# Performance work log

Hardware: AMD Instinct MI355X
Metric: run time of the kernel (lower is better)

The kernel has to match this reference:

```python
import jax, jax.numpy as jnp
import numpy as np

N = 51200      # total nodes
E = 1638400    # total edges (avg degree 32)
G = 512        # graphs in batch
IN = 16        # input node features
H = 4          # heads
C = 32         # channels per head
HC = H * C     # 128, concat output width
SLOPE = 0.2    # LeakyReLU negative slope
BN_EPS = 1e-5


def _glorot(k, shape, fan):
    return jax.random.normal(k, shape, jnp.float32) / np.sqrt(fan).astype(np.float32)


def setup_inputs() -> dict:
    key = jax.random.key(0)
    ks = jax.random.split(key, 32)
    inp = {}
    inp['x'] = jax.random.normal(ks[0], (N, IN), jnp.float32)
    inp['edge_index'] = jax.random.randint(ks[1], (2, E), 0, N)
    inp['batch'] = jnp.sort(jax.random.randint(ks[2], (N,), 0, G))
    # GATv2 layer 1 (IN -> H*C)
    inp['l1_Wl'] = _glorot(ks[3], (IN, HC), IN)
    inp['l1_bl'] = jnp.zeros((HC,), jnp.float32)
    inp['l1_Wr'] = _glorot(ks[4], (IN, HC), IN)
    inp['l1_br'] = jnp.zeros((HC,), jnp.float32)
    inp['l1_att'] = _glorot(ks[5], (H, C), C)
    inp['l1_bias'] = jnp.zeros((HC,), jnp.float32)
    # GATv2 layer 2 (HC -> H*C)
    inp['l2_Wl'] = _glorot(ks[6], (HC, HC), HC)
    inp['l2_bl'] = jnp.zeros((HC,), jnp.float32)
    inp['l2_Wr'] = _glorot(ks[7], (HC, HC), HC)
    inp['l2_br'] = jnp.zeros((HC,), jnp.float32)
    inp['l2_att'] = _glorot(ks[8], (H, C), C)
    inp['l2_bias'] = jnp.zeros((HC,), jnp.float32)
    # MLP head (HC -> HC -> HC -> 2) with BatchNorm (eval mode, running stats 0/1)
    inp['fc1_W'] = _glorot(ks[9], (HC, HC), HC)
    inp['fc1_b'] = jnp.zeros((HC,), jnp.float32)
    inp['bn1_g'] = jnp.ones((HC,), jnp.float32)
    inp['bn1_b'] = jnp.zeros((HC,), jnp.float32)
    inp['fc2_W'] = _glorot(ks[10], (HC, HC), HC)
    inp['fc2_b'] = jnp.zeros((HC,), jnp.float32)
    inp['bn2_g'] = jnp.ones((HC,), jnp.float32)
    inp['bn2_b'] = jnp.zeros((HC,), jnp.float32)
    inp['fc3_W'] = _glorot(ks[11], (HC, 2), HC)
    inp['fc3_b'] = jnp.zeros((2,), jnp.float32)
    return inp


def gatv2_conv(x, src, dst, Wl, bl, Wr, br, att, bias):
    # PyG GATv2Conv (share_weights=False, concat=True), eval mode (no dropout).
    xl = (x @ Wl + bl).reshape(-1, H, C)  # source transform  [N,H,C]
    xr = (x @ Wr + br).reshape(-1, H, C)  # target transform  [N,H,C]
    e = jax.nn.leaky_relu(xl[src] + xr[dst], SLOPE)   # [E,H,C]
    score = jnp.einsum('ehc,hc->eh', e, att)          # [E,H]
    # segment softmax over edges sharing the same target node
    m = jax.ops.segment_max(score, dst, num_segments=N)
    ex = jnp.exp(score - m[dst])
    denom = jax.ops.segment_sum(ex, dst, num_segments=N)
    alpha = ex / (denom[dst] + 1e-16)                 # [E,H]
    out = jax.ops.segment_sum(xl[src] * alpha[:, :, None], dst, num_segments=N)
    return out.reshape(-1, HC) + bias


def reference(x, edge_index, batch,
              l1_Wl, l1_bl, l1_Wr, l1_br, l1_att, l1_bias,
              l2_Wl, l2_bl, l2_Wr, l2_br, l2_att, l2_bias,
              fc1_W, fc1_b, bn1_g, bn1_b,
              fc2_W, fc2_b, bn2_g, bn2_b,
              fc3_W, fc3_b):
    src, dst = edge_index[0], edge_index[1]
    h = jax.nn.relu(gatv2_conv(x, src, dst, l1_Wl, l1_bl, l1_Wr, l1_br, l1_att, l1_bias))
    h = jax.nn.relu(gatv2_conv(h, src, dst, l2_Wl, l2_bl, l2_Wr, l2_br, l2_att, l2_bias))
    # global mean pool over graphs
    s = jax.ops.segment_sum(h, batch, num_segments=G)
    cnt = jax.ops.segment_sum(jnp.ones((N,), h.dtype), batch, num_segments=G)
    g = s / jnp.maximum(cnt, 1.0)[:, None]            # [G,HC]
    # MLP head; BatchNorm1d in eval mode with running_mean=0, running_var=1
    def bn(z, gamma, beta):
        return z * (gamma / np.sqrt(1.0 + BN_EPS).astype(np.float32)) + beta
    g = jax.nn.relu(bn(g @ fc1_W + fc1_b, bn1_g, bn1_b))
    g = jax.nn.relu(bn(g @ fc2_W + fc2_b, bn2_g, bn2_b))
    return g @ fc3_W + fc3_b                          # [G,2]
```

## Files before the change

### kernel.cpp

```cpp
#include <hip/hip_runtime.h>
#include <math.h>

#define NN 51200
#define EE 1638400
#define GG 512
#define INF 16
#define HCC 128
#define NB 400
#define TILE 4096
#define NBLK (NN / 4)

typedef float vf2 __attribute__((ext_vector_type(2)));
#define FMA2 __builtin_elementwise_fma
#define MIN2 __builtin_elementwise_min
#define MAX2 __builtin_elementwise_max


__device__ __forceinline__ int wave_incl_scan(int v, int lane) {
#pragma unroll
    for (int d = 1; d < 64; d <<= 1) {
        int y = __shfl_up(v, d);
        if (lane >= d) v += y;
    }
    return v;
}

__global__ __launch_bounds__(256) void k_hist(const int* __restrict__ ei,
                                              int* __restrict__ bcnt) {
    __shared__ int h[NB];
    for (int i = threadIdx.x; i < NB; i += 256) h[i] = 0;
    __syncthreads();
    int e0 = blockIdx.x * TILE;
#pragma unroll
    for (int s = 0; s < 16; s++) {
        int d = ei[EE + e0 + s * 256 + threadIdx.x];
        atomicAdd(&h[d >> 7], 1);
    }
    __syncthreads();
    for (int i = threadIdx.x; i < NB; i += 256)
        if (h[i]) atomicAdd(&bcnt[i], h[i]);
}

__global__ __launch_bounds__(512) void k_scan2(const int* __restrict__ bcnt,
                                               int* __restrict__ bbase,
                                               int* __restrict__ gcur,
                                               int* __restrict__ rowptr) {
    __shared__ int sc[512];
    int t = threadIdx.x;
    int v = (t < NB) ? bcnt[t] : 0;
    sc[t] = v;
    __syncthreads();
    for (int off = 1; off < 512; off <<= 1) {
        int u = (t >= off) ? sc[t - off] : 0;
        __syncthreads();
        sc[t] += u;
        __syncthreads();
    }
    if (t < NB) { int ex = sc[t] - v; bbase[t] = ex; gcur[t] = ex; }
    if (t == 0) { bbase[NB] = EE; rowptr[NN] = EE; }
}

__global__ __launch_bounds__(512) void k_binlin1(const int* __restrict__ ei,
                                                 int* __restrict__ gcur,
                                                 unsigned* __restrict__ binned,
                                                 const float* __restrict__ x,
                                                 const float* __restrict__ Wl,
                                                 const float* __restrict__ bl,
                                                 const float* __restrict__ Wr,
                                                 const float* __restrict__ br,
                                                 float* __restrict__ xl,
                                                 float* __restrict__ xr) {
    __shared__ int h[512];
    __shared__ int lexcl[NB], lcur[NB], baseg[NB];
    __shared__ unsigned stage[TILE];
    __shared__ int wsum[8];
    __shared__ float sx[4][INF];
    int t = threadIdx.x;
    if (blockIdx.x < NB) {
        int lane = t & 63, w = t >> 6;
        h[t] = 0;
        __syncthreads();
        int e0 = blockIdx.x * TILE;
        int sv[8], dv[8];
#pragma unroll
        for (int s = 0; s < 8; s++) {
            int e = e0 + s * 512 + t;
            sv[s] = ei[e];
            dv[s] = ei[EE + e];
            atomicAdd(&h[dv[s] >> 7], 1);
        }
        __syncthreads();
        int myh = h[t];
        int incl = wave_incl_scan(myh, lane);
        if (lane == 63) wsum[w] = incl;
        __syncthreads();
        int woff = 0;
        for (int i = 0; i < w; i++) woff += wsum[i];
        incl += woff;
        if (t < NB) {
            int ex = incl - myh;
            lexcl[t] = ex;
            lcur[t] = ex;
            baseg[t] = atomicAdd(&gcur[t], myh);
        }
        __syncthreads();
#pragma unroll
        for (int s = 0; s < 8; s++) {
            int b = dv[s] >> 7;
            int r = atomicAdd(&lcur[b], 1);
            stage[r] = (unsigned)sv[s] | ((unsigned)dv[s] << 16);
        }
        __syncthreads();
#pragma unroll
        for (int s = 0; s < 8; s++) {
            int idx = s * 512 + t;
            unsigned p = stage[idx];
            int b = (int)(p >> 23);
            binned[baseg[b] + idx - lexcl[b]] = p;
        }
    } else {
        int bid = blockIdx.x - NB;
        int j = t & 127;
        int ty = t >> 7;
        int row = bid * 4 + ty;
        if (t < 64) {
            sx[t >> 4][t & 15] = x[(size_t)(bid * 4 + (t >> 4)) * INF + (t & 15)];
        }
        __syncthreads();
        float al = bl[j], ar = br[j];
#pragma unroll
        for (int k = 0; k < INF; k++) {
            float xv = sx[ty][k];
            al = fmaf(xv, Wl[k * HCC + j], al);
            ar = fmaf(xv, Wr[k * HCC + j], ar);
        }
        size_t s = ((size_t)(j >> 5) * NN + row) * 32 + (j & 31);
        xl[s] = al;
        xr[s] = ar;
    }
}

__global__ __launch_bounds__(256) void k_csr(const unsigned* __restrict__ binned,
                                             const int* __restrict__ bbase,
                                             int* __restrict__ rowptr,
                                             int* __restrict__ col) {
    int b = blockIdx.x;
    int base = bbase[b];
    int cnt = bbase[b + 1] - base;
    __shared__ int nh[1024], ncur[1024];
    __shared__ int wsum[4];
    int t = threadIdx.x;
    int lane = t & 63, w = t >> 6;
#pragma unroll
    for (int i = 0; i < 4; i++) nh[t + 256 * i] = 0;
    __syncthreads();
    for (int e = t; e < cnt; e += 256) {
        unsigned p = binned[base + e];
        unsigned src = p & 0xFFFFu;
        int key = (int)(((p >> 16) & 127u) << 3) | (int)(src >> 13);
        atomicAdd(&nh[key], 1);
    }
    __syncthreads();
    int c0 = nh[4 * t + 0], c1 = nh[4 * t + 1], c2 = nh[4 * t + 2], c3 = nh[4 * t + 3];
    int tot = ((c0 + c1) + (c2 + c3));
    int incl = wave_incl_scan(tot, lane);
    if (lane == 63) wsum[w] = incl;
    __syncthreads();
    int woff = 0;
    for (int i = 0; i < w; i++) woff += wsum[i];
    int tex = incl + woff - tot;
    ncur[4 * t + 0] = base + tex;
    ncur[4 * t + 1] = base + tex + c0;
    ncur[4 * t + 2] = base + tex + c0 + c1;
    ncur[4 * t + 3] = base + tex + c0 + c1 + c2;
    if ((t & 1) == 0) rowptr[(b << 7) + (t >> 1)] = base + tex;
    __syncthreads();
    for (int e = t; e < cnt; e += 256) {
        unsigned p = binned[base + e];
        unsigned src = p & 0xFFFFu;
        int key = (int)(((p >> 16) & 127u) << 3) | (int)(src >> 13);
        int r = atomicAdd(&ncur[key], 1);
        col[r] = (int)src;
    }
}

#define AST2 36
#define BST 260
__global__ __launch_bounds__(512) void k_lin2(const float* __restrict__ hin,
                                              const float* __restrict__ Wl,
                                              const float* __restrict__ bl,
                                              const float* __restrict__ Wr,
                                              const float* __restrict__ br,
                                              float* __restrict__ outl,
                                              float* __restrict__ outr) {
    __shared__ float As[128 * AST2];
    __shared__ float Bs[32 * BST];
    const int tid = threadIdx.x;
    const int cx = tid & 31;
    const int cy = tid >> 5;
    const int r0 = blockIdx.x * 128;

    vf2 accL[8][2], accR[8][2];
#pragma unroll
    for (int j = 0; j < 8; j++)
#pragma unroll
        for (int i = 0; i < 2; i++) {
            accL[j][i] = (vf2){0.f, 0.f};
            accR[j][i] = (vf2){0.f, 0.f};
        }

    for (int k0 = 0; k0 < HCC; k0 += 32) {
#pragma unroll
        for (int s = 0; s < 2; s++) {
            int f = tid + 512 * s;
            int row = f >> 3;
            int kk = (f & 7) * 4;
            float4 v = *(const float4*)(hin + (size_t)(r0 + row) * HCC + k0 + kk);
            *(float4*)&As[row * AST2 + kk] = v;
        }
#pragma unroll
        for (int s = 0; s < 4; s++) {
            int g = tid + 512 * s;
            int kr = g >> 6;
            int c4 = g & 63;
            const float* srcp = (c4 < 32)
                ? (Wl + (size_t)(k0 + kr) * HCC + c4 * 4)
                : (Wr + (size_t)(k0 + kr) * HCC + (c4 - 32) * 4);
            *(float4*)&Bs[kr * BST + c4 * 4] = *(const float4*)srcp;
        }
        __syncthreads();
#pragma unroll
        for (int k = 0; k < 32; k += 4) {
            float4 a4[8];
#pragma unroll
            for (int j = 0; j < 8; ++j)
                a4[j] = *(const float4*)&As[(cy + 16 * j) * AST2 + k];
#pragma unroll
            for (int kk = 0; kk < 4; ++kk) {
                float4 b4l = *(const float4*)&Bs[(k + kk) * BST + cx * 4];
                float4 b4r = *(const float4*)&Bs[(k + kk) * BST + 128 + cx * 4];
                const vf2 bl0 = {b4l.x, b4l.y}, bl1 = {b4l.z, b4l.w};
                const vf2 br0 = {b4r.x, b4r.y}, br1 = {b4r.z, b4r.w};
#pragma unroll
                for (int j = 0; j < 8; ++j) {
                    float a = ((const float*)&a4[j])[kk];
                    const vf2 av = {a, a};
                    accL[j][0] = FMA2(av, bl0, accL[j][0]);
                    accL[j][1] = FMA2(av, bl1, accL[j][1]);
                    accR[j][0] = FMA2(av, br0, accR[j][0]);
                    accR[j][1] = FMA2(av, br1, accR[j][1]);
                }
            }
        }
        __syncthreads();
    }
    float4 bv_l = *(const float4*)(bl + cx * 4);
    float4 bv_r = *(const float4*)(br + cx * 4);
    const size_t plane = (size_t)(cx >> 3) * NN * 32;
    const int off = (cx & 7) * 4;
#pragma unroll
    for (int j = 0; j < 8; ++j) {
        int row = r0 + cy + 16 * j;
        float4 o;
        o.x = accL[j][0].x + bv_l.x;
        o.y = accL[j][0].y + bv_l.y;
        o.z = accL[j][1].x + bv_l.z;
        o.w = accL[j][1].y + bv_l.w;
        *(float4*)(outl + plane + (size_t)row * 32 + off) = o;
        o.x = accR[j][0].x + bv_r.x;
        o.y = accR[j][0].y + bv_r.y;
        o.z = accR[j][1].x + bv_r.z;
        o.w = accR[j][1].y + bv_r.w;
        *(float4*)(outr + plane + (size_t)row * 32 + off) = o;
    }
}

__global__ __launch_bounds__(256) void k_attn(const int* __restrict__ rowptr,
                                              const int* __restrict__ col,
                                              const float* __restrict__ xl,
                                              const float* __restrict__ xr,
                                              const float* __restrict__ att,
                                              const float* __restrict__ bias,
                                              float* __restrict__ hout) {
    const int wave = threadIdx.x >> 6;
    const int lane = threadIdx.x & 63;
    const int sub = lane >> 3;
    const int hl = (lane >> 2) & 1;
    const int hq = lane & 3;
    const int pair = blockIdx.x / NBLK;
    const int n = (blockIdx.x - pair * NBLK) * 4 + wave;
    const int head = 2 * pair + hl;

    const float* xlh = xl + (size_t)head * NN * 32;
    const float* xrp = xr + ((size_t)head * NN + n) * 32 + hq * 8;
    const float4 xrv0 = *(const float4*)(xrp);
    const float4 xrv1 = *(const float4*)(xrp + 4);
    const float4 at0 = *(const float4*)(att + head * 32 + hq * 8);
    const float4 at1 = *(const float4*)(att + head * 32 + hq * 8 + 4);
    const vf2 xr01 = {xrv0.x, xrv0.y}, xr23 = {xrv0.z, xrv0.w};
    const vf2 xr45 = {xrv1.x, xrv1.y}, xr67 = {xrv1.z, xrv1.w};
    const vf2 at01 = {at0.x, at0.y}, at23 = {at0.z, at0.w};
    const vf2 at45 = {at1.x, at1.y}, at67 = {at1.z, at1.w};
    const vf2 Z2 = {0.f, 0.f}, C2 = {0.2f, 0.2f};
    const unsigned choff = (unsigned)hq * 32u;

    const int base = rowptr[n];
    const int deg = rowptr[n + 1] - base;

    float m = -INFINITY, l = 0.f;
    vf2 a01 = Z2, a23 = Z2, a45 = Z2, a67 = Z2;

    for (int i0 = 0; i0 < deg; i0 += 64) {
        int mye = 0;
        if (i0 + lane < deg) mye = col[base + i0 + lane];
        const int cnt = min(64, deg - i0);
        const int events = (cnt + 15) >> 4;
        for (int g = 0; g < events; ++g) {
            float4 v0[2], v1[2];
            float p[2];
#pragma unroll
            for (int k = 0; k < 2; ++k) {
                const int src = __shfl(mye, 16 * g + 8 * k + sub);
                const unsigned voff = ((unsigned)src << 7) + choff;
                v0[k] = *(const float4*)((const char*)xlh + voff);
                v1[k] = *(const float4*)((const char*)xlh + voff + 16);
            }
#pragma unroll
            for (int k = 0; k < 2; ++k) {
                const vf2 v01 = {v0[k].x, v0[k].y}, v23 = {v0[k].z, v0[k].w};
                const vf2 v45 = {v1[k].x, v1[k].y}, v67 = {v1[k].z, v1[k].w};
                vf2 e, kk, p2;
                e = v01 + xr01; kk = FMA2(C2, MIN2(e, Z2), MAX2(e, Z2)); p2 = kk * at01;
                e = v23 + xr23; kk = FMA2(C2, MIN2(e, Z2), MAX2(e, Z2)); p2 = FMA2(kk, at23, p2);
                e = v45 + xr45; kk = FMA2(C2, MIN2(e, Z2), MAX2(e, Z2)); p2 = FMA2(kk, at45, p2);
                e = v67 + xr67; kk = FMA2(C2, MIN2(e, Z2), MAX2(e, Z2)); p2 = FMA2(kk, at67, p2);
                float pp = p2.x + p2.y;
                pp += __shfl_xor(pp, 1);
                pp += __shfl_xor(pp, 2);
                if ((16 * g + 8 * k + sub) >= cnt) pp = -INFINITY;
                p[k] = pp;
            }
            float pm = fmaxf(p[0], p[1]);
            pm = fmaxf(pm, __shfl_xor(pm, 8));
            pm = fmaxf(pm, __shfl_xor(pm, 16));
            pm = fmaxf(pm, __shfl_xor(pm, 32));
            const float mn = fmaxf(m, pm);
            const float sc = __expf(m - mn);
            const float w0 = __expf(p[0] - mn);
            const float w1 = __expf(p[1] - mn);
            l = fmaf(l, sc, w0 + w1);
            const vf2 S = {sc, sc}, W0 = {w0, w0}, W1 = {w1, w1};
            const vf2 u01 = {v0[0].x, v0[0].y}, u23 = {v0[0].z, v0[0].w};
            const vf2 u45 = {v1[0].x, v1[0].y}, u67 = {v1[0].z, v1[0].w};
            const vf2 t01 = {v0[1].x, v0[1].y}, t23 = {v0[1].z, v0[1].w};
            const vf2 t45 = {v1[1].x, v1[1].y}, t67 = {v1[1].z, v1[1].w};
            a01 = FMA2(W1, t01, FMA2(W0, u01, a01 * S));
            a23 = FMA2(W1, t23, FMA2(W0, u23, a23 * S));
            a45 = FMA2(W1, t45, FMA2(W0, u45, a45 * S));
            a67 = FMA2(W1, t67, FMA2(W0, u67, a67 * S));
            m = mn;
        }
    }
    l += __shfl_xor(l, 8);
    l += __shfl_xor(l, 16);
    l += __shfl_xor(l, 32);
    float af[8] = {a01.x, a01.y, a23.x, a23.y, a45.x, a45.y, a67.x, a67.y};
#pragma unroll
    for (int i = 0; i < 8; i++) {
        af[i] += __shfl_xor(af[i], 8);
        af[i] += __shfl_xor(af[i], 16);
        af[i] += __shfl_xor(af[i], 32);
    }
    const float inv = 1.f / (l + 1e-16f);
    if (sub == 0) {
        const float4 b0 = *(const float4*)(bias + head * 32 + hq * 8);
        const float4 b1 = *(const float4*)(bias + head * 32 + hq * 8 + 4);
        float4 o0, o1;
        o0.x = fmaxf(fmaf(af[0], inv, b0.x), 0.f);
        o0.y = fmaxf(fmaf(af[1], inv, b0.y), 0.f);
        o0.z = fmaxf(fmaf(af[2], inv, b0.z), 0.f);
        o0.w = fmaxf(fmaf(af[3], inv, b0.w), 0.f);
        o1.x = fmaxf(fmaf(af[4], inv, b1.x), 0.f);
        o1.y = fmaxf(fmaf(af[5], inv, b1.y), 0.f);
        o1.z = fmaxf(fmaf(af[6], inv, b1.z), 0.f);
        o1.w = fmaxf(fmaf(af[7], inv, b1.w), 0.f);
        float* hp = hout + (size_t)n * HCC + head * 32 + hq * 8;
        *(float4*)(hp) = o0;
        *(float4*)(hp + 4) = o1;
    }
}

__global__ __launch_bounds__(128) void k_head(const float* __restrict__ h,
                                              const int* __restrict__ batch,
                                              const float* __restrict__ fc1W, const float* __restrict__ fc1b,
                                              const float* __restrict__ bn1g, const float* __restrict__ bn1b,
                                              const float* __restrict__ fc2W, const float* __restrict__ fc2b,
                                              const float* __restrict__ bn2g, const float* __restrict__ bn2b,
                                              const float* __restrict__ fc3W, const float* __restrict__ fc3b,
                                              float* __restrict__ out) {
    int g = blockIdx.x;
    int j = threadIdx.x;
    __shared__ float buf[HCC], buf2[HCC];
    int lo = 0, hi = NN;
    while (lo < hi) { int mid = (lo + hi) >> 1; if (batch[mid] < g) lo = mid + 1; else hi = mid; }
    int s = lo;
    lo = 0; hi = NN;
    while (lo < hi) { int mid = (lo + hi) >> 1; if (batch[mid] < g + 1) lo = mid + 1; else hi = mid; }
    int e = lo;
    float s0 = 0.f, s1 = 0.f, s2 = 0.f, s3 = 0.f;
    int n = s;
    for (; n + 3 < e; n += 4) {
        s0 += h[(size_t)n * HCC + j];
        s1 += h[(size_t)(n + 1) * HCC + j];
        s2 += h[(size_t)(n + 2) * HCC + j];
        s3 += h[(size_t)(n + 3) * HCC + j];
    }
    for (; n < e; n++) s0 += h[(size_t)n * HCC + j];
    float sum = (s0 + s1) + (s2 + s3);
    float cnt = (float)(e - s);
    buf[j] = sum / fmaxf(cnt, 1.0f);
    __syncthreads();
    const float SQ = 1.00000499998749994f;
    float a = fc1b[j];
    for (int k = 0; k < HCC; k++) a = fmaf(buf[k], fc1W[k * HCC + j], a);
    a = fmaf(a, bn1g[j] / SQ, bn1b[j]);
    a = fmaxf(a, 0.f);
    buf2[j] = a;
    __syncthreads();
    a = fc2b[j];
    for (int k = 0; k < HCC; k++) a = fmaf(buf2[k], fc2W[k * HCC + j], a);
    a = fmaf(a, bn2g[j] / SQ, bn2b[j]);
    a = fmaxf(a, 0.f);
    buf[j] = a;
    __syncthreads();
    if (j < 2) {
        float o = fc3b[j];
        for (int k = 0; k < HCC; k++) o = fmaf(buf[k], fc3W[k * 2 + j], o);
        out[g * 2 + j] = o;
    }
}

extern "C" void kernel_launch(void* const* d_in, const int* in_sizes, int n_in,
                              void* d_out, int out_size, void* d_ws, size_t ws_size,
                              hipStream_t stream) {
    const float* x      = (const float*)d_in[0];
    const int*   ei     = (const int*)d_in[1];
    const int*   batch  = (const int*)d_in[2];
    const float* l1_Wl  = (const float*)d_in[3];
    const float* l1_bl  = (const float*)d_in[4];
    const float* l1_Wr  = (const float*)d_in[5];
    const float* l1_br  = (const float*)d_in[6];
    const float* l1_att = (const float*)d_in[7];
    const float* l1_bias= (const float*)d_in[8];
    const float* l2_Wl  = (const float*)d_in[9];
    const float* l2_bl  = (const float*)d_in[10];
    const float* l2_Wr  = (const float*)d_in[11];
    const float* l2_br  = (const float*)d_in[12];
    const float* l2_att = (const float*)d_in[13];
    const float* l2_bias= (const float*)d_in[14];
    const float* fc1_W  = (const float*)d_in[15];
    const float* fc1_b  = (const float*)d_in[16];
    const float* bn1_g  = (const float*)d_in[17];
    const float* bn1_b  = (const float*)d_in[18];
    const float* fc2_W  = (const float*)d_in[19];
    const float* fc2_b  = (const float*)d_in[20];
    const float* bn2_g  = (const float*)d_in[21];
    const float* bn2_b  = (const float*)d_in[22];
    const float* fc3_W  = (const float*)d_in[23];
    const float* fc3_b  = (const float*)d_in[24];
    float* out = (float*)d_out;

    float* xl = (float*)d_ws;
    float* xr = xl + (size_t)NN * HCC;
    float* h  = xr + (size_t)NN * HCC;
    int* rowptr = (int*)(h + (size_t)NN * HCC);
    int* col    = rowptr + (NN + 1);
    int* bcnt   = col + EE;
    int* bbase  = bcnt + NB;
    int* gcur   = bbase + (NB + 1);
    unsigned* binned = (unsigned*)h;

    hipMemsetAsync(bcnt, 0, NB * sizeof(int), stream);
    k_hist<<<EE / TILE, 256, 0, stream>>>(ei, bcnt);
    k_scan2<<<1, 512, 0, stream>>>(bcnt, bbase, gcur, rowptr);
    k_binlin1<<<NB + NN / 4, 512, 0, stream>>>(ei, gcur, binned,
                                               x, l1_Wl, l1_bl, l1_Wr, l1_br, xl, xr);
    k_csr<<<NB, 256, 0, stream>>>(binned, bbase, rowptr, col);

    k_attn<<<2 * NBLK, 256, 0, stream>>>(rowptr, col, xl, xr, l1_att, l1_bias, h);

    k_lin2<<<NN / 128, 512, 0, stream>>>(h, l2_Wl, l2_bl, l2_Wr, l2_br, xl, xr);
    k_attn<<<2 * NBLK, 256, 0, stream>>>(rowptr, col, xl, xr, l2_att, l2_bias, h);

    k_head<<<GG, 128, 0, stream>>>(h, batch, fc1_W, fc1_b, bn1_g, bn1_b,
                                   fc2_W, fc2_b, bn2_g, bn2_b, fc3_W, fc3_b, out);
}
```

Baseline: 474.6 us.

## Run layer-2 linear on bf16x3 MFMA with weights pre-split in binning kernel

Replaces the FP32 SIMT GEMM for the layer-2 source/target transforms with MFMA 16x16x32 bf16 instructions. Accuracy is kept close to FP32 by splitting each operand into hi/lo bf16 parts and summing three products. The weight split and swizzle into MFMA fragment layout happen in 8 extra blocks appended to the binning kernel, so k_lin2 reads pre-packed B fragments. The cost is a small precision change and per-element strided scalar output stores, in exchange for much higher matrix throughput on a GEMM of about 51200x128x256.

```diff
diff --git a/kernel.cpp b/kernel.cpp
--- a/kernel.cpp
+++ b/kernel.cpp
@@ -11,6 +11,8 @@
 #define NBLK (NN / 4)
 
 typedef float vf2 __attribute__((ext_vector_type(2)));
+typedef short v8s __attribute__((ext_vector_type(8)));
+typedef float v4f __attribute__((ext_vector_type(4)));
 #define FMA2 __builtin_elementwise_fma
 #define MIN2 __builtin_elementwise_min
 #define MAX2 __builtin_elementwise_max
@@ -23,6 +25,12 @@
         if (lane >= d) v += y;
     }
     return v;
+}
+
+__device__ __forceinline__ unsigned short bf16_rtne(float f) {
+    unsigned u = __builtin_bit_cast(unsigned, f);
+    unsigned r = u + 0x7FFFu + ((u >> 16) & 1u);
+    return (unsigned short)(r >> 16);
 }
 
 __global__ __launch_bounds__(256) void k_hist(const int* __restrict__ ei,
@@ -69,7 +77,11 @@
                                                  const float* __restrict__ Wr,
                                                  const float* __restrict__ br,
                                                  float* __restrict__ xl,
-                                                 float* __restrict__ xr) {
+                                                 float* __restrict__ xr,
+                                                 const float* __restrict__ W2l,
+                                                 const float* __restrict__ W2r,
+                                                 unsigned short* __restrict__ Bhi,
+                                                 unsigned short* __restrict__ Blo) {
     __shared__ int h[512];
     __shared__ int lexcl[NB], lcur[NB], baseg[NB];
     __shared__ unsigned stage[TILE];
@@ -118,7 +130,7 @@
             int b = (int)(p >> 23);
             binned[baseg[b] + idx - lexcl[b]] = p;
         }
-    } else {
+    } else if (blockIdx.x < NB + NN / 4) {
         int bid = blockIdx.x - NB;
         int j = t & 127;
         int ty = t >> 7;
@@ -137,6 +149,27 @@
         size_t s = ((size_t)(j >> 5) * NN + row) * 32 + (j & 31);
         xl[s] = al;
         xr[s] = ar;
+    } else {
+        int gt = (blockIdx.x - NB - NN / 4) * 512 + t;
+        int ks = gt >> 10;
+        int rem = gt & 1023;
+        int nt = rem >> 6;
+        int lane = rem & 63;
+        int n = nt * 16 + (lane & 15);
+        int kbase = ks * 32 + (lane >> 4) * 8;
+        const float* src = (n < 128) ? (W2l + n) : (W2r + n - 128);
+        unsigned short hi8[8], lo8[8];
+#pragma unroll
+        for (int j = 0; j < 8; j++) {
+            float v = src[(size_t)(kbase + j) * HCC];
+            unsigned short hb = bf16_rtne(v);
+            float hf = __builtin_bit_cast(float, (unsigned)hb << 16);
+            hi8[j] = hb;
+            lo8[j] = bf16_rtne(v - hf);
+        }
+        size_t idx = (size_t)gt * 8;
+#pragma unroll
+        for (int j = 0; j < 8; j++) { Bhi[idx + j] = hi8[j]; Blo[idx + j] = lo8[j]; }
     }
 }
 
@@ -184,94 +217,61 @@
     }
 }
 
-#define AST2 36
-#define BST 260
-__global__ __launch_bounds__(512) void k_lin2(const float* __restrict__ hin,
-                                              const float* __restrict__ Wl,
+__global__ __launch_bounds__(256) void k_lin2(const float* __restrict__ hin,
+                                              const unsigned short* __restrict__ Bhi,
+                                              const unsigned short* __restrict__ Blo,
                                               const float* __restrict__ bl,
-                                              const float* __restrict__ Wr,
                                               const float* __restrict__ br,
                                               float* __restrict__ outl,
                                               float* __restrict__ outr) {
-    __shared__ float As[128 * AST2];
-    __shared__ float Bs[32 * BST];
     const int tid = threadIdx.x;
-    const int cx = tid & 31;
-    const int cy = tid >> 5;
-    const int r0 = blockIdx.x * 128;
-
-    vf2 accL[8][2], accR[8][2];
-#pragma unroll
-    for (int j = 0; j < 8; j++)
-#pragma unroll
-        for (int i = 0; i < 2; i++) {
-            accL[j][i] = (vf2){0.f, 0.f};
-            accR[j][i] = (vf2){0.f, 0.f};
-        }
-
-    for (int k0 = 0; k0 < HCC; k0 += 32) {
-#pragma unroll
-        for (int s = 0; s < 2; s++) {
-            int f = tid + 512 * s;
-            int row = f >> 3;
-            int kk = (f & 7) * 4;
-            float4 v = *(const float4*)(hin + (size_t)(r0 + row) * HCC + k0 + kk);
-            *(float4*)&As[row * AST2 + kk] = v;
-        }
-#pragma unroll
-        for (int s = 0; s < 4; s++) {
-            int g = tid + 512 * s;
-            int kr = g >> 6;
-            int c4 = g & 63;
-            const float* srcp = (c4 < 32)
-                ? (Wl + (size_t)(k0 + kr) * HCC + c4 * 4)
-                : (Wr + (size_t)(k0 + kr) * HCC + (c4 - 32) * 4);
-            *(float4*)&Bs[kr * BST + c4 * 4] = *(const float4*)srcp;
-        }
-        __syncthreads();
-#pragma unroll
-        for (int k = 0; k < 32; k += 4) {
-            float4 a4[8];
-#pragma unroll
-            for (int j = 0; j < 8; ++j)
-                a4[j] = *(const float4*)&As[(cy + 16 * j) * AST2 + k];
-#pragma unroll
-            for (int kk = 0; kk < 4; ++kk) {
-                float4 b4l = *(const float4*)&Bs[(k + kk) * BST + cx * 4];
-                float4 b4r = *(const float4*)&Bs[(k + kk) * BST + 128 + cx * 4];
-                const vf2 bl0 = {b4l.x, b4l.y}, bl1 = {b4l.z, b4l.w};
-                const vf2 br0 = {b4r.x, b4r.y}, br1 = {b4r.z, b4r.w};
-#pragma unroll
-                for (int j = 0; j < 8; ++j) {
-                    float a = ((const float*)&a4[j])[kk];
-                    const vf2 av = {a, a};
-                    accL[j][0] = FMA2(av, bl0, accL[j][0]);
-                    accL[j][1] = FMA2(av, bl1, accL[j][1]);
-                    accR[j][0] = FMA2(av, br0, accR[j][0]);
-                    accR[j][1] = FMA2(av, br1, accR[j][1]);
-                }
-            }
-        }
-        __syncthreads();
-    }
-    float4 bv_l = *(const float4*)(bl + cx * 4);
-    float4 bv_r = *(const float4*)(br + cx * 4);
-    const size_t plane = (size_t)(cx >> 3) * NN * 32;
-    const int off = (cx & 7) * 4;
-#pragma unroll
-    for (int j = 0; j < 8; ++j) {
-        int row = r0 + cy + 16 * j;
-        float4 o;
-        o.x = accL[j][0].x + bv_l.x;
-        o.y = accL[j][0].y + bv_l.y;
-        o.z = accL[j][1].x + bv_l.z;
-        o.w = accL[j][1].y + bv_l.w;
-        *(float4*)(outl + plane + (size_t)row * 32 + off) = o;
-        o.x = accR[j][0].x + bv_r.x;
-        o.y = accR[j][0].y + bv_r.y;
-        o.z = accR[j][1].x + bv_r.z;
-        o.w = accR[j][1].y + bv_r.w;
-        *(float4*)(outr + plane + (size_t)row * 32 + off) = o;
+    const int wv = tid >> 6;
+    const int lane = tid & 63;
+    const int m = lane & 15;
+    const int quad = lane >> 4;
+    const int r0 = blockIdx.x * 64 + wv * 16;
+    const float* arow = hin + (size_t)(r0 + m) * HCC + quad * 8;
+    const v8s* bh = (const v8s*)Bhi;
+    const v8s* bo = (const v8s*)Blo;
+
+    v4f acc[16];
+#pragma unroll
+    for (int nt = 0; nt < 16; nt++) acc[nt] = (v4f){0.f, 0.f, 0.f, 0.f};
+
+#pragma unroll
+    for (int ks = 0; ks < 4; ks++) {
+        const float4 av0 = *(const float4*)(arow + ks * 32);
+        const float4 av1 = *(const float4*)(arow + ks * 32 + 4);
+        const float af[8] = {av0.x, av0.y, av0.z, av0.w, av1.x, av1.y, av1.z, av1.w};
+        v8s ahi, alo;
+#pragma unroll
+        for (int e = 0; e < 8; e++) {
+            unsigned short hb = bf16_rtne(af[e]);
+            float hf = __builtin_bit_cast(float, (unsigned)hb << 16);
+            ahi[e] = (short)hb;
+            alo[e] = (short)bf16_rtne(af[e] - hf);
+        }
+        const int base = ks * 16 * 64 + lane;
+#pragma unroll
+        for (int nt = 0; nt < 16; nt++) {
+            v8s bhv = bh[base + nt * 64];
+            v8s blv = bo[base + nt * 64];
+            acc[nt] = __builtin_amdgcn_mfma_f32_16x16x32_bf16(ahi, bhv, acc[nt], 0, 0, 0);
+            acc[nt] = __builtin_amdgcn_mfma_f32_16x16x32_bf16(ahi, blv, acc[nt], 0, 0, 0);
+            acc[nt] = __builtin_amdgcn_mfma_f32_16x16x32_bf16(alo, bhv, acc[nt], 0, 0, 0);
+        }
+    }
+#pragma unroll
+    for (int nt = 0; nt < 16; nt++) {
+        int n = nt * 16 + m;
+        int c = n & 127;
+        float bv = (n < 128) ? bl[c] : br[c];
+        float* outp = ((n < 128) ? outl : outr) + (size_t)(c >> 5) * NN * 32 + (c & 31);
+#pragma unroll
+        for (int r = 0; r < 4; r++) {
+            int row = r0 + quad * 4 + r;
+            outp[(size_t)row * 32] = acc[nt][r] + bv;
+        }
     }
 }
 
@@ -478,18 +478,22 @@
     int* bcnt   = col + EE;
     int* bbase  = bcnt + NB;
     int* gcur   = bbase + (NB + 1);
+    uintptr_t bp = ((uintptr_t)(gcur + NB) + 15) & ~(uintptr_t)15;
+    unsigned short* Bhi = (unsigned short*)bp;
+    unsigned short* Blo = Bhi + 32768;
     unsigned* binned = (unsigned*)h;
 
     hipMemsetAsync(bcnt, 0, NB * sizeof(int), stream);
     k_hist<<<EE / TILE, 256, 0, stream>>>(ei, bcnt);
     k_scan2<<<1, 512, 0, stream>>>(bcnt, bbase, gcur, rowptr);
-    k_binlin1<<<NB + NN / 4, 512, 0, stream>>>(ei, gcur, binned,
-                                               x, l1_Wl, l1_bl, l1_Wr, l1_br, xl, xr);
+    k_binlin1<<<NB + NN / 4 + 8, 512, 0, stream>>>(ei, gcur, binned,
+                                                   x, l1_Wl, l1_bl, l1_Wr, l1_br, xl, xr,
+                                                   l2_Wl, l2_Wr, Bhi, Blo);
     k_csr<<<NB, 256, 0, stream>>>(binned, bbase, rowptr, col);
 
     k_attn<<<2 * NBLK, 256, 0, stream>>>(rowptr, col, xl, xr, l1_att, l1_bias, h);
 
-    k_lin2<<<NN / 128, 512, 0, stream>>>(h, l2_Wl, l2_bl, l2_Wr, l2_br, xl, xr);
+    k_lin2<<<NN / 64, 256, 0, stream>>>(h, Bhi, Blo, l2_bl, l2_br, xl, xr);
     k_attn<<<2 * NBLK, 256, 0, stream>>>(rowptr, col, xl, xr, l2_att, l2_bias, h);
 
     k_head<<<GG, 128, 0, stream>>>(h, batch, fc1_W, fc1_b, bn1_g, bn1_b,
```

New measurement: 449.4 us. 1.06x faster.
